# Kernel optimization log

Hardware: AMD Instinct MI355X
Metric: run time of the kernel (lower is better)

Reference implementation:

```python
import math
import jax, jax.numpy as jnp
import numpy as np

HEADS = 8
DIM = 512
HEAD_SIZE = DIM // HEADS  # 64


def setup_inputs() -> dict:
    key = jax.random.key(0)
    ks = jax.random.split(key, 5)
    b, nh, nw, t, d = 16, 16, 16, 16, DIM
    x = jax.random.normal(ks[0], (b, nh, nw, t, d), dtype=jnp.float32)
    s = 1.0 / math.sqrt(d)
    Wq = jax.random.normal(ks[1], (d, d), dtype=jnp.float32) * s
    Wk = jax.random.normal(ks[2], (d, d), dtype=jnp.float32) * s
    Wv = jax.random.normal(ks[3], (d, d), dtype=jnp.float32) * s
    Wo = jax.random.normal(ks[4], (d, d), dtype=jnp.float32) * s
    z = jnp.zeros((d,), dtype=jnp.float32)
    return {"x": x, "Wq": Wq, "bq": z, "Wk": Wk, "bk": z, "Wv": Wv, "bv": z, "Wo": Wo, "bo": z}


def _split_heads(t):
    # [b, n1, n2, T, D] -> [b, n1, n2, H, T, hs]
    b, n1, n2, T, _ = t.shape
    return t.reshape(b, n1, n2, T, HEADS, HEAD_SIZE).transpose(0, 1, 2, 4, 3, 5)


def reference(x, Wq, bq, Wk, bk, Wv, bv, Wo, bo):
    q = _split_heads(x @ Wq + bq)
    k = _split_heads(x @ Wk + bk)
    v = _split_heads(x @ Wv + bv)
    # windowed attention scores: [b, n1, n2, H, T, T]
    scores = jnp.einsum('bnmhtd,bnmhsd->bnmhts', q, k) / math.sqrt(HEAD_SIZE)
    probs = jax.nn.sigmoid(scores)  # NOTE: elementwise sigmoid, not softmax
    ctx = jnp.einsum('bnmhts,bnmhsd->bnmhtd', probs, v)
    b, n1, n2, H, T, hs = ctx.shape
    ctx = ctx.transpose(0, 1, 2, 4, 3, 5).reshape(b, n1, n2, T, H * hs)
    return ctx @ Wo + bo
```

## Files before the change

### kernel.cpp

```cpp
#include <hip/hip_runtime.h>
#include <hip/hip_bf16.h>

typedef float f32x4 __attribute__((ext_vector_type(4)));
typedef __bf16 bf16x8 __attribute__((ext_vector_type(8)));
typedef unsigned short u16x4 __attribute__((ext_vector_type(4)));
typedef unsigned short u16x8 __attribute__((ext_vector_type(8)));

__device__ __forceinline__ unsigned short f2bf(float f) {
  union { float f; unsigned u; } x; x.f = f;
  unsigned r = x.u + 0x7FFFu + ((x.u >> 16) & 1u);
  return (unsigned short)(r >> 16);
}
__device__ __forceinline__ float bf2f(unsigned short u) {
  union { unsigned u; float f; } x; x.u = ((unsigned)u) << 16;
  return x.f;
}

__device__ __forceinline__ void gl16(const void* g, void* l) {
  __builtin_amdgcn_global_load_lds(
      (const __attribute__((address_space(1))) unsigned*)g,
      (__attribute__((address_space(3))) unsigned*)l, 16, 0, 0);
}

__global__ __launch_bounds__(256) void prep_wt(const float* __restrict__ Wq,
                                               const float* __restrict__ Wk,
                                               const float* __restrict__ Wv,
                                               const float* __restrict__ Wo,
                                               unsigned short* __restrict__ WT) {
  __shared__ unsigned short ts[64][65];
  const float* W = (blockIdx.z == 0) ? Wq : (blockIdx.z == 1) ? Wk
                   : (blockIdx.z == 2) ? Wv : Wo;
  const int t = threadIdx.x;
  const int kbase = blockIdx.y * 64;
  const int nbase = blockIdx.x * 64;
  for (int i = 0; i < 16; ++i) {
    int idx = i * 256 + t;
    int r = idx >> 6, c = idx & 63;
    ts[r][c] = f2bf(W[(size_t)(kbase + r) * 512 + nbase + c]);
  }
  __syncthreads();
  unsigned short* dst = WT + (size_t)blockIdx.z * 512 * 512;
  for (int i = 0; i < 16; ++i) {
    int idx = i * 256 + t;
    int nn = idx >> 6, kk = idx & 63;
    dst[(size_t)(nbase + nn) * 512 + kbase + kk] = ts[kk][nn];
  }
}

__global__ void prep_bias(const float* __restrict__ bq, const float* __restrict__ bk,
                          const float* __restrict__ bv, float* __restrict__ biasc) {
  int i = blockIdx.x * 256 + threadIdx.x;
  if (i < 512) biasc[i] = bq[i];
  else if (i < 1024) biasc[i] = bk[i - 512];
  else if (i < 1536) biasc[i] = bv[i - 1024];
}

__global__ __launch_bounds__(256) void convert_x(const float* __restrict__ x,
                                                 unsigned short* __restrict__ xb,
                                                 long long n8) {
  long long i = (long long)blockIdx.x * 256 + threadIdx.x;
  const long long stride = (long long)gridDim.x * 256;
  for (; i < n8; i += stride) {
    f32x4 a = *reinterpret_cast<const f32x4*>(&x[i * 8]);
    f32x4 b = *reinterpret_cast<const f32x4*>(&x[i * 8 + 4]);
    u16x8 o;
    o[0] = f2bf(a[0]); o[1] = f2bf(a[1]); o[2] = f2bf(a[2]); o[3] = f2bf(a[3]);
    o[4] = f2bf(b[0]); o[5] = f2bf(b[1]); o[6] = f2bf(b[2]); o[7] = f2bf(b[3]);
    *reinterpret_cast<u16x8*>(&xb[i * 8]) = o;
  }
}

template <typename CT>
__global__ __launch_bounds__(512, 2) void gemm256(
    const unsigned short* __restrict__ A, int lda,
    const unsigned short* __restrict__ BT,
    CT* __restrict__ C, int ldc,
    const float* __restrict__ bias, int NB) {
  __shared__ alignas(16) unsigned short As[2][16384];
  __shared__ alignas(16) unsigned short Bs[2][16384];
  const int t = threadIdx.x;
  const int lane = t & 63;
  const int w = t >> 6;
  const int wm = w >> 2, wn = w & 3;

  const int nwg = gridDim.x;
  const int cpx = nwg >> 3;
  const int wg = (blockIdx.x & 7) * cpx + (blockIdx.x >> 3);
  const int n0 = (wg % NB) * 256;
  const int m0 = (wg / NB) * 256;

  const int sr = lane >> 3;
  const int sg = ((lane & 7) ^ sr) << 3;
  const unsigned short* gA = A + (size_t)(m0 + w * 8 + sr) * lda + sg;
  const unsigned short* gB = BT + (size_t)(n0 + w * 8 + sr) * 512 + sg;
  const int lw = w * 512;

#define STAGE_A(kt, h, b)                                                   \
  { const unsigned short* g_ = gA + (size_t)(h) * 128 * lda + (kt) * 64;    \
    unsigned short* l_ = &As[b][(h) * 8192 + lw];                           \
    gl16(g_, l_); gl16(g_ + (size_t)64 * lda, l_ + 4096); }
#define STAGE_B(kt, h, b)                                                   \
  { const unsigned short* g_ = gB + (size_t)(h) * 128 * 512 + (kt) * 64;    \
    unsigned short* l_ = &Bs[b][(h) * 8192 + lw];                           \
    gl16(g_, l_); gl16(g_ + (size_t)64 * 512, l_ + 4096); }

  const int fr = lane & 15;
  const int fg = lane >> 4;
  const int fx = lane & 7;
  auto readA = [&](int b, int mi, int kf) -> bf16x8 {
    return *reinterpret_cast<const bf16x8*>(
        &As[b][(wm * 128 + mi * 16 + fr) * 64 + ((((kf << 2) + fg) ^ fx) << 3)]);
  };
  auto readB = [&](int b, int ni, int kf) -> bf16x8 {
    return *reinterpret_cast<const bf16x8*>(
        &Bs[b][(wn * 64 + ni * 16 + fr) * 64 + ((((kf << 2) + fg) ^ fx) << 3)]);
  };

  f32x4 acc[8][4];
#pragma unroll
  for (int i = 0; i < 8; ++i)
#pragma unroll
    for (int j = 0; j < 4; ++j) acc[i][j] = (f32x4){0.f, 0.f, 0.f, 0.f};
  bf16x8 bfr[4][2];

#define PHASE(b, q, READB, STAGES, VM)                                       \
  {                                                                          \
    bf16x8 a0_ = readA(b, 2 * (q), 0), a1_ = readA(b, 2 * (q), 1);           \
    bf16x8 a2_ = readA(b, 2 * (q) + 1, 0), a3_ = readA(b, 2 * (q) + 1, 1);   \
    if (READB) {                                                             \
      _Pragma("unroll") for (int ni = 0; ni < 4; ++ni) {                     \
        bfr[ni][0] = readB(b, ni, 0);                                        \
        bfr[ni][1] = readB(b, ni, 1);                                        \
      }                                                                      \
    }                                                                        \
    STAGES;                                                                  \
    if ((VM) == 4) asm volatile("s_waitcnt vmcnt(4)" ::: "memory");          \
    if ((VM) == 0) asm volatile("s_waitcnt vmcnt(0)" ::: "memory");          \
    __builtin_amdgcn_s_barrier();                                            \
    asm volatile("s_waitcnt lgkmcnt(0)" ::: "memory");                       \
    __builtin_amdgcn_sched_barrier(0);                                       \
    __builtin_amdgcn_s_setprio(1);                                           \
    _Pragma("unroll") for (int ni = 0; ni < 4; ++ni) {                       \
      acc[2 * (q)][ni] = __builtin_amdgcn_mfma_f32_16x16x32_bf16(            \
          a0_, bfr[ni][0], acc[2 * (q)][ni], 0, 0, 0);                       \
      acc[2 * (q)][ni] = __builtin_amdgcn_mfma_f32_16x16x32_bf16(            \
          a1_, bfr[ni][1], acc[2 * (q)][ni], 0, 0, 0);                       \
      acc[2 * (q) + 1][ni] = __builtin_amdgcn_mfma_f32_16x16x32_bf16(        \
          a2_, bfr[ni][0], acc[2 * (q) + 1][ni], 0, 0, 0);                   \
      acc[2 * (q) + 1][ni] = __builtin_amdgcn_mfma_f32_16x16x32_bf16(        \
          a3_, bfr[ni][1], acc[2 * (q) + 1][ni], 0, 0, 0);                   \
    }                                                                        \
    __builtin_amdgcn_s_setprio(0);                                           \
    __builtin_amdgcn_s_barrier();                                            \
  }

  STAGE_B(0, 0, 0); STAGE_B(0, 1, 0);
  STAGE_A(0, 0, 0); STAGE_A(0, 1, 0);
  STAGE_B(1, 0, 1); STAGE_B(1, 1, 1);
  asm volatile("s_waitcnt vmcnt(4)" ::: "memory");
  __builtin_amdgcn_s_barrier();

#pragma unroll
  for (int i = 0; i < 4; ++i) {
    const bool s2 = (i < 3);
    const int vmA = s2 ? 4 : 0;
    const int vmB = s2 ? 4 : 0;
    PHASE(0, 0, true,  { STAGE_A(2 * i + 1, 0, 1) }, -1);
    PHASE(0, 1, false, { STAGE_A(2 * i + 1, 1, 1) if (s2) STAGE_B(2 * i + 2, 0, 0) }, -1);
    PHASE(0, 2, false, { if (s2) STAGE_B(2 * i + 2, 1, 0) }, -1);
    PHASE(0, 3, false, {}, vmA);
    PHASE(1, 0, true,  { if (s2) STAGE_A(2 * i + 2, 0, 0) }, -1);
    PHASE(1, 1, false, { if (s2) STAGE_A(2 * i + 2, 1, 0) }, -1);
    PHASE(1, 2, false, { if (s2) STAGE_B(2 * i + 3, 0, 1) }, -1);
    PHASE(1, 3, false, { if (s2) STAGE_B(2 * i + 3, 1, 1) }, vmB);
  }
#undef PHASE
#undef STAGE_A
#undef STAGE_B

#pragma unroll
  for (int ni = 0; ni < 4; ++ni) {
    int col = n0 + wn * 64 + ni * 16 + fr;
    float bc = bias[col];
#pragma unroll
    for (int mi = 0; mi < 8; ++mi) {
      int rowb = m0 + wm * 128 + mi * 16 + fg * 4;
#pragma unroll
      for (int r = 0; r < 4; ++r) {
        float v = acc[mi][ni][r] + bc;
        if constexpr (sizeof(CT) == 2)
          C[(size_t)(rowb + r) * ldc + col] = (CT)f2bf(v);
        else
          C[(size_t)(rowb + r) * ldc + col] = (CT)v;
      }
    }
  }
}

__global__ __launch_bounds__(256) void attn_kernel(unsigned short* __restrict__ QKV) {
  __shared__ alignas(16) unsigned short qs[16][1544];
  __shared__ unsigned short ps[8][16][16];
  const int t = threadIdx.x;
  const size_t base = (size_t)blockIdx.x * 16;

  {
    int row = t >> 4;
    int cb = (t & 15) * 96;
    const unsigned short* src = QKV + (base + row) * 1536;
#pragma unroll
    for (int i = 0; i < 24; ++i) {
      int c = cb + i * 4;
      *reinterpret_cast<u16x4*>(&qs[row][c]) = *reinterpret_cast<const u16x4*>(&src[c]);
    }
  }
  __syncthreads();

  const int tq = t >> 4;
  const int tk = t & 15;
#pragma unroll
  for (int h = 0; h < 8; ++h) {
    float acc = 0.f;
#pragma unroll
    for (int dc = 0; dc < 64; dc += 8) {
      u16x8 q8 = *reinterpret_cast<const u16x8*>(&qs[tq][h * 64 + dc]);
      u16x8 k8 = *reinterpret_cast<const u16x8*>(&qs[tk][512 + h * 64 + dc]);
#pragma unroll
      for (int j = 0; j < 8; ++j) acc += bf2f(q8[j]) * bf2f(k8[j]);
    }
    ps[h][tq][tk] = f2bf(1.0f / (1.0f + __expf(-acc * 0.125f)));
  }
  __syncthreads();

  const int row = t >> 4;
  const int cb4 = (t & 15) * 4;
  unsigned short* dst = QKV + (base + row) * 1536 + 1024;
#pragma unroll
  for (int h = 0; h < 8; ++h) {
    f32x4 acc = (f32x4){0.f, 0.f, 0.f, 0.f};
#pragma unroll
    for (int s = 0; s < 16; ++s) {
      float p = bf2f(ps[h][row][s]);
      u16x4 v4 = *reinterpret_cast<const u16x4*>(&qs[s][1024 + h * 64 + cb4]);
      acc[0] += p * bf2f(v4[0]); acc[1] += p * bf2f(v4[1]);
      acc[2] += p * bf2f(v4[2]); acc[3] += p * bf2f(v4[3]);
    }
    u16x4 o4;
    o4[0] = f2bf(acc[0]); o4[1] = f2bf(acc[1]); o4[2] = f2bf(acc[2]); o4[3] = f2bf(acc[3]);
    *reinterpret_cast<u16x4*>(&dst[h * 64 + cb4]) = o4;
  }
}

extern "C" void kernel_launch(void* const* d_in, const int* in_sizes, int n_in,
                              void* d_out, int out_size, void* d_ws, size_t ws_size,
                              hipStream_t stream) {
  const float* x  = (const float*)d_in[0];
  const float* Wq = (const float*)d_in[1];
  const float* bq = (const float*)d_in[2];
  const float* Wk = (const float*)d_in[3];
  const float* bk = (const float*)d_in[4];
  const float* Wv = (const float*)d_in[5];
  const float* bv = (const float*)d_in[6];
  const float* Wo = (const float*)d_in[7];
  const float* bo = (const float*)d_in[8];
  float* out = (float*)d_out;

  const int M = 65536;
  char* ws = (char*)d_ws;
  unsigned short* WT = (unsigned short*)ws;
  float* biasc = (float*)(ws + (size_t)2048 * 512 * 2);
  const long long prep_bytes = (long long)2048 * 512 * 2 + 8192;

  prep_wt<<<dim3(8, 8, 4), 256, 0, stream>>>(Wq, Wk, Wv, Wo, WT);
  prep_bias<<<6, 256, 0, stream>>>(bq, bk, bv, biasc);

  long long avail = (long long)ws_size - prep_bytes;
  int chunk_rows = 65536;
  while (chunk_rows > 2048 && (long long)chunk_rows * 4096 > avail) chunk_rows >>= 1;
  const int nchunks = M / chunk_rows;

  unsigned short* Xb  = (unsigned short*)(ws + prep_bytes);
  unsigned short* QKV = Xb + (size_t)chunk_rows * 512;

  for (int c = 0; c < nchunks; ++c) {
    const size_t row0 = (size_t)c * chunk_rows;
    const int mt = chunk_rows / 256;
    convert_x<<<2048, 256, 0, stream>>>(x + row0 * 512, Xb,
                                        (long long)chunk_rows * 64);
    gemm256<unsigned short><<<mt * 6, 512, 0, stream>>>(
        Xb, 512, WT, QKV, 1536, biasc, 6);
    attn_kernel<<<chunk_rows / 16, 256, 0, stream>>>(QKV);
    gemm256<float><<<mt * 2, 512, 0, stream>>>(
        QKV + 1024, 1536, WT + (size_t)1536 * 512, out + row0 * 512, 512, bo, 2);
  }
}
```

Before: 340.7 us.

## Fuse fp32-to-bf16 conversion of x into QKV GEMM A-tile staging

Drops the separate convert_x kernel. The QKV GEMM now loads fp32 x tiles into registers, converts them to bf16 and writes them swizzled into LDS, interleaved with the existing B-tile global_load_lds pipeline. This removes one full write and read of the bf16 copy of x. The change also swaps the MFMA operand order so the accumulator is transposed, which lets the epilogue do vectorized 4-wide stores and bias loads, and the workspace need per row drops. The costs are more register pressure and VGPR round-trips for A, and the A loads (about 128 MB of fp32) are now read directly inside the GEMM.

```diff
diff --git a/kernel.cpp b/kernel.cpp
--- a/kernel.cpp
+++ b/kernel.cpp
@@ -3,6 +3,7 @@
 
 typedef float f32x4 __attribute__((ext_vector_type(4)));
 typedef __bf16 bf16x8 __attribute__((ext_vector_type(8)));
+typedef __bf16 bf16x4 __attribute__((ext_vector_type(4)));
 typedef unsigned short u16x4 __attribute__((ext_vector_type(4)));
 typedef unsigned short u16x8 __attribute__((ext_vector_type(8)));
 
@@ -55,29 +56,13 @@
   else if (i < 1536) biasc[i] = bv[i - 1024];
 }
 
-__global__ __launch_bounds__(256) void convert_x(const float* __restrict__ x,
-                                                 unsigned short* __restrict__ xb,
-                                                 long long n8) {
-  long long i = (long long)blockIdx.x * 256 + threadIdx.x;
-  const long long stride = (long long)gridDim.x * 256;
-  for (; i < n8; i += stride) {
-    f32x4 a = *reinterpret_cast<const f32x4*>(&x[i * 8]);
-    f32x4 b = *reinterpret_cast<const f32x4*>(&x[i * 8 + 4]);
-    u16x8 o;
-    o[0] = f2bf(a[0]); o[1] = f2bf(a[1]); o[2] = f2bf(a[2]); o[3] = f2bf(a[3]);
-    o[4] = f2bf(b[0]); o[5] = f2bf(b[1]); o[6] = f2bf(b[2]); o[7] = f2bf(b[3]);
-    *reinterpret_cast<u16x8*>(&xb[i * 8]) = o;
-  }
-}
-
-template <typename CT>
+template <typename AT, typename CT>
 __global__ __launch_bounds__(512, 2) void gemm256(
-    const unsigned short* __restrict__ A, int lda,
+    const AT* __restrict__ A, int lda,
     const unsigned short* __restrict__ BT,
     CT* __restrict__ C, int ldc,
     const float* __restrict__ bias, int NB) {
-  __shared__ alignas(16) unsigned short As[2][16384];
-  __shared__ alignas(16) unsigned short Bs[2][16384];
+  __shared__ alignas(16) unsigned short pool[65536];
   const int t = threadIdx.x;
   const int lane = t & 63;
   const int w = t >> 6;
@@ -91,29 +76,54 @@
 
   const int sr = lane >> 3;
   const int sg = ((lane & 7) ^ sr) << 3;
-  const unsigned short* gA = A + (size_t)(m0 + w * 8 + sr) * lda + sg;
   const unsigned short* gB = BT + (size_t)(n0 + w * 8 + sr) * 512 + sg;
   const int lw = w * 512;
 
-#define STAGE_A(kt, h, b)                                                   \
-  { const unsigned short* g_ = gA + (size_t)(h) * 128 * lda + (kt) * 64;    \
-    unsigned short* l_ = &As[b][(h) * 8192 + lw];                           \
+#define SB(kt, h, b)                                                        \
+  { const unsigned short* g_ = gB + (size_t)(h) * 128 * 512 + (kt) * 64;    \
+    unsigned short* l_ = &pool[32768 + (b) * 16384 + (h) * 8192 + lw];      \
+    gl16(g_, l_); gl16(g_ + (size_t)64 * 512, l_ + 4096); }
+
+  const unsigned short* gAu = nullptr;
+  if constexpr (sizeof(AT) == 2)
+    gAu = (const unsigned short*)A + (size_t)(m0 + w * 8 + sr) * lda + sg;
+#define SA(kt, h, b)                                                        \
+  { const unsigned short* g_ = gAu + (size_t)(h) * 128 * lda + (kt) * 64;   \
+    unsigned short* l_ = &pool[(b) * 16384 + (h) * 8192 + lw];              \
     gl16(g_, l_); gl16(g_ + (size_t)64 * lda, l_ + 4096); }
-#define STAGE_B(kt, h, b)                                                   \
-  { const unsigned short* g_ = gB + (size_t)(h) * 128 * 512 + (kt) * 64;    \
-    unsigned short* l_ = &Bs[b][(h) * 8192 + lw];                           \
-    gl16(g_, l_); gl16(g_ + (size_t)64 * 512, l_ + 4096); }
+
+  f32x4 ar[4][2];
+  const int seg = t & 7;
+  const int rbase = t >> 3;
+  const float* gAf = nullptr;
+  if constexpr (sizeof(AT) == 4)
+    gAf = (const float*)A + (size_t)(m0 + rbase) * lda + seg * 8;
+#define LA(kt, u)                                                           \
+  { const float* g_ = gAf + (size_t)(u) * 64 * lda + (kt) * 64;             \
+    ar[u][0] = *reinterpret_cast<const f32x4*>(g_);                         \
+    ar[u][1] = *reinterpret_cast<const f32x4*>(g_ + 4); }
+#define WA(u, b)                                                            \
+  { int row_ = rbase + (u) * 64;                                            \
+    bf16x8 pk_;                                                             \
+    _Pragma("unroll") for (int j_ = 0; j_ < 4; ++j_) {                      \
+      pk_[j_] = (__bf16)ar[u][0][j_];                                       \
+      pk_[4 + j_] = (__bf16)ar[u][1][j_];                                   \
+    }                                                                       \
+    *reinterpret_cast<bf16x8*>(                                             \
+        &pool[(b) * 16384 + row_ * 64 + ((seg ^ (row_ & 7)) << 3)]) = pk_; }
 
   const int fr = lane & 15;
   const int fg = lane >> 4;
   const int fx = lane & 7;
   auto readA = [&](int b, int mi, int kf) -> bf16x8 {
     return *reinterpret_cast<const bf16x8*>(
-        &As[b][(wm * 128 + mi * 16 + fr) * 64 + ((((kf << 2) + fg) ^ fx) << 3)]);
+        &pool[(b) * 16384 + (wm * 128 + mi * 16 + fr) * 64 +
+              ((((kf << 2) + fg) ^ fx) << 3)]);
   };
   auto readB = [&](int b, int ni, int kf) -> bf16x8 {
     return *reinterpret_cast<const bf16x8*>(
-        &Bs[b][(wn * 64 + ni * 16 + fr) * 64 + ((((kf << 2) + fg) ^ fx) << 3)]);
+        &pool[32768 + (b) * 16384 + (wn * 64 + ni * 16 + fr) * 64 +
+              ((((kf << 2) + fg) ^ fx) << 3)]);
   };
 
   f32x4 acc[8][4];
@@ -142,56 +152,78 @@
     __builtin_amdgcn_s_setprio(1);                                           \
     _Pragma("unroll") for (int ni = 0; ni < 4; ++ni) {                       \
       acc[2 * (q)][ni] = __builtin_amdgcn_mfma_f32_16x16x32_bf16(            \
-          a0_, bfr[ni][0], acc[2 * (q)][ni], 0, 0, 0);                       \
+          bfr[ni][0], a0_, acc[2 * (q)][ni], 0, 0, 0);                       \
+      acc[2 * (q) + 1][ni] = __builtin_amdgcn_mfma_f32_16x16x32_bf16(        \
+          bfr[ni][0], a2_, acc[2 * (q) + 1][ni], 0, 0, 0);                   \
+    }                                                                        \
+    _Pragma("unroll") for (int ni = 0; ni < 4; ++ni) {                       \
       acc[2 * (q)][ni] = __builtin_amdgcn_mfma_f32_16x16x32_bf16(            \
-          a1_, bfr[ni][1], acc[2 * (q)][ni], 0, 0, 0);                       \
+          bfr[ni][1], a1_, acc[2 * (q)][ni], 0, 0, 0);                       \
       acc[2 * (q) + 1][ni] = __builtin_amdgcn_mfma_f32_16x16x32_bf16(        \
-          a2_, bfr[ni][0], acc[2 * (q) + 1][ni], 0, 0, 0);                   \
-      acc[2 * (q) + 1][ni] = __builtin_amdgcn_mfma_f32_16x16x32_bf16(        \
-          a3_, bfr[ni][1], acc[2 * (q) + 1][ni], 0, 0, 0);                   \
+          bfr[ni][1], a3_, acc[2 * (q) + 1][ni], 0, 0, 0);                   \
     }                                                                        \
     __builtin_amdgcn_s_setprio(0);                                           \
     __builtin_amdgcn_s_barrier();                                            \
   }
 
-  STAGE_B(0, 0, 0); STAGE_B(0, 1, 0);
-  STAGE_A(0, 0, 0); STAGE_A(0, 1, 0);
-  STAGE_B(1, 0, 1); STAGE_B(1, 1, 1);
-  asm volatile("s_waitcnt vmcnt(4)" ::: "memory");
-  __builtin_amdgcn_s_barrier();
-
-#pragma unroll
-  for (int i = 0; i < 4; ++i) {
-    const bool s2 = (i < 3);
-    const int vmA = s2 ? 4 : 0;
-    const int vmB = s2 ? 4 : 0;
-    PHASE(0, 0, true,  { STAGE_A(2 * i + 1, 0, 1) }, -1);
-    PHASE(0, 1, false, { STAGE_A(2 * i + 1, 1, 1) if (s2) STAGE_B(2 * i + 2, 0, 0) }, -1);
-    PHASE(0, 2, false, { if (s2) STAGE_B(2 * i + 2, 1, 0) }, -1);
-    PHASE(0, 3, false, {}, vmA);
-    PHASE(1, 0, true,  { if (s2) STAGE_A(2 * i + 2, 0, 0) }, -1);
-    PHASE(1, 1, false, { if (s2) STAGE_A(2 * i + 2, 1, 0) }, -1);
-    PHASE(1, 2, false, { if (s2) STAGE_B(2 * i + 3, 0, 1) }, -1);
-    PHASE(1, 3, false, { if (s2) STAGE_B(2 * i + 3, 1, 1) }, vmB);
+  if constexpr (sizeof(AT) == 4) {
+    LA(0, 0) LA(0, 1) LA(0, 2) LA(0, 3)
+    SB(0, 0, 0) SB(0, 1, 0) SB(1, 0, 1) SB(1, 1, 1)
+    WA(0, 0) WA(1, 0) WA(2, 0) WA(3, 0)
+    asm volatile("s_waitcnt vmcnt(4) lgkmcnt(0)" ::: "memory");
+    __builtin_amdgcn_s_barrier();
+#pragma unroll
+    for (int i = 0; i < 4; ++i) {
+      const bool s2 = (i < 3);
+      PHASE(0, 0, true,  { LA(2 * i + 1, 0) LA(2 * i + 1, 1) }, -1);
+      PHASE(0, 1, false, { LA(2 * i + 1, 2) LA(2 * i + 1, 3) if (s2) SB(2 * i + 2, 0, 0) }, -1);
+      PHASE(0, 2, false, { WA(0, 1) WA(1, 1) if (s2) SB(2 * i + 2, 1, 0) }, -1);
+      PHASE(0, 3, false, { WA(2, 1) WA(3, 1) }, s2 ? 4 : 0);
+      PHASE(1, 0, true,  { if (s2) { LA(2 * i + 2, 0) LA(2 * i + 2, 1) } }, -1);
+      PHASE(1, 1, false, { if (s2) { LA(2 * i + 2, 2) LA(2 * i + 2, 3) SB(2 * i + 3, 0, 1) } }, -1);
+      PHASE(1, 2, false, { if (s2) { WA(0, 0) WA(1, 0) SB(2 * i + 3, 1, 1) } }, -1);
+      PHASE(1, 3, false, { if (s2) { WA(2, 0) WA(3, 0) } }, s2 ? 4 : 0);
+    }
+  } else {
+    SB(0, 0, 0) SB(0, 1, 0)
+    SA(0, 0, 0) SA(0, 1, 0)
+    SB(1, 0, 1) SB(1, 1, 1)
+    asm volatile("s_waitcnt vmcnt(4)" ::: "memory");
+    __builtin_amdgcn_s_barrier();
+#pragma unroll
+    for (int i = 0; i < 4; ++i) {
+      const bool s2 = (i < 3);
+      PHASE(0, 0, true,  { SA(2 * i + 1, 0, 1) }, -1);
+      PHASE(0, 1, false, { SA(2 * i + 1, 1, 1) if (s2) SB(2 * i + 2, 0, 0) }, -1);
+      PHASE(0, 2, false, { if (s2) SB(2 * i + 2, 1, 0) }, -1);
+      PHASE(0, 3, false, {}, s2 ? 4 : 0);
+      PHASE(1, 0, true,  { if (s2) SA(2 * i + 2, 0, 0) }, -1);
+      PHASE(1, 1, false, { if (s2) SA(2 * i + 2, 1, 0) }, -1);
+      PHASE(1, 2, false, { if (s2) SB(2 * i + 3, 0, 1) }, -1);
+      PHASE(1, 3, false, { if (s2) SB(2 * i + 3, 1, 1) }, s2 ? 4 : 0);
+    }
   }
 #undef PHASE
-#undef STAGE_A
-#undef STAGE_B
-
-#pragma unroll
-  for (int ni = 0; ni < 4; ++ni) {
-    int col = n0 + wn * 64 + ni * 16 + fr;
-    float bc = bias[col];
-#pragma unroll
-    for (int mi = 0; mi < 8; ++mi) {
-      int rowb = m0 + wm * 128 + mi * 16 + fg * 4;
-#pragma unroll
-      for (int r = 0; r < 4; ++r) {
-        float v = acc[mi][ni][r] + bc;
-        if constexpr (sizeof(CT) == 2)
-          C[(size_t)(rowb + r) * ldc + col] = (CT)f2bf(v);
-        else
-          C[(size_t)(rowb + r) * ldc + col] = (CT)v;
+#undef SA
+#undef SB
+#undef LA
+#undef WA
+
+#pragma unroll
+  for (int mi = 0; mi < 8; ++mi) {
+    const size_t m = (size_t)(m0 + wm * 128 + mi * 16 + fr);
+#pragma unroll
+    for (int ni = 0; ni < 4; ++ni) {
+      const int nb = n0 + wn * 64 + ni * 16 + fg * 4;
+      f32x4 b4 = *reinterpret_cast<const f32x4*>(&bias[nb]);
+      if constexpr (sizeof(CT) == 2) {
+        u16x4 o;
+#pragma unroll
+        for (int r = 0; r < 4; ++r) o[r] = f2bf(acc[mi][ni][r] + b4[r]);
+        *reinterpret_cast<u16x4*>(&C[m * ldc + nb]) = o;
+      } else {
+        f32x4 o = acc[mi][ni] + b4;
+        *reinterpret_cast<f32x4*>(&C[m * ldc + nb]) = o;
       }
     }
   }
@@ -275,21 +307,18 @@
 
   long long avail = (long long)ws_size - prep_bytes;
   int chunk_rows = 65536;
-  while (chunk_rows > 2048 && (long long)chunk_rows * 4096 > avail) chunk_rows >>= 1;
+  while (chunk_rows > 2048 && (long long)chunk_rows * 3072 > avail) chunk_rows >>= 1;
   const int nchunks = M / chunk_rows;
 
-  unsigned short* Xb  = (unsigned short*)(ws + prep_bytes);
-  unsigned short* QKV = Xb + (size_t)chunk_rows * 512;
+  unsigned short* QKV = (unsigned short*)(ws + prep_bytes);
 
   for (int c = 0; c < nchunks; ++c) {
     const size_t row0 = (size_t)c * chunk_rows;
     const int mt = chunk_rows / 256;
-    convert_x<<<2048, 256, 0, stream>>>(x + row0 * 512, Xb,
-                                        (long long)chunk_rows * 64);
-    gemm256<unsigned short><<<mt * 6, 512, 0, stream>>>(
-        Xb, 512, WT, QKV, 1536, biasc, 6);
+    gemm256<float, unsigned short><<<mt * 6, 512, 0, stream>>>(
+        x + row0 * 512, 512, WT, QKV, 1536, biasc, 6);
     attn_kernel<<<chunk_rows / 16, 256, 0, stream>>>(QKV);
-    gemm256<float><<<mt * 2, 512, 0, stream>>>(
+    gemm256<unsigned short, float><<<mt * 2, 512, 0, stream>>>(
         QKV + 1024, 1536, WT + (size_t)1536 * 512, out + row0 * 512, 512, bo, 2);
   }
 }
```

Result: faster. 327.0 us (-4.0%).
